# Kernel optimization log

Hardware: AMD Instinct MI355X
Metric: run time of the kernel (lower is better)

The kernel has to match this reference:

```python
import jax, jax.numpy as jnp
import numpy as np

B, S, D, H, HD = 2, 2048, 1024, 16, 64


def setup_inputs() -> dict:
    key = jax.random.key(0)
    ks = jax.random.split(key, 5)
    sc = 1.0 / np.sqrt(D)  # lecun-normal-ish scale for kernels
    return {
        "x": jax.random.normal(ks[0], (B, S, D), jnp.float32),
        "Wq": jax.random.normal(ks[1], (D, H, HD), jnp.float32) * sc,
        "bq": jnp.zeros((H, HD), jnp.float32),
        "Wk": jax.random.normal(ks[2], (D, H, HD), jnp.float32) * sc,
        "bk": jnp.zeros((H, HD), jnp.float32),
        "Wv": jax.random.normal(ks[3], (D, H, HD), jnp.float32) * sc,
        "bv": jnp.zeros((H, HD), jnp.float32),
        "Wo": jax.random.normal(ks[4], (H, HD, D), jnp.float32) * (1.0 / np.sqrt(H * HD)),
        "bo": jnp.zeros((D,), jnp.float32),
    }


def reference(x, Wq, bq, Wk, bk, Wv, bv, Wo, bo):
    # QKV projections: [B,S,D] x [D,H,Hd] -> [B,S,H,Hd]
    q = jnp.einsum("bsd,dhk->bshk", x, Wq) + bq
    k = jnp.einsum("bsd,dhk->bshk", x, Wk) + bk
    v = jnp.einsum("bsd,dhk->bshk", x, Wv) + bv
    depth = q.shape[-1]
    q = q / jnp.sqrt(jnp.asarray(depth, q.dtype))
    # attention weights [B,H,Sq,Sk]
    attn = jnp.einsum("bqhd,bkhd->bhqk", q, k)
    attn = jax.nn.softmax(attn, axis=-1)
    # weighted values [B,Sq,H,Hd]
    out = jnp.einsum("bhqk,bkhd->bqhd", attn, v)
    # output projection back to d_model
    return jnp.einsum("bqhd,hdm->bqm", out, Wo) + bo
```

## Files before the change

kernel.cpp:

```cpp
#include <hip/hip_runtime.h>


typedef __attribute__((ext_vector_type(8))) short short8;
typedef __attribute__((ext_vector_type(4))) float float4v;
typedef __attribute__((ext_vector_type(16))) float f32x16;
typedef __attribute__((ext_vector_type(2))) int int2v;

__device__ __forceinline__ void async16(void* lds, const void* g) {
  __builtin_amdgcn_global_load_lds(
      (__attribute__((address_space(1))) void*)(g),
      (__attribute__((address_space(3))) void*)(lds), 16, 0, 0);
}

__device__ __forceinline__ short f2bf(float f) {
  union { float f; unsigned u; } v;
  v.f = f;
  unsigned r = v.u + 0x7fffu + ((v.u >> 16) & 1u);
  return (short)(r >> 16);
}

#if __has_builtin(__builtin_amdgcn_cvt_pk_bf16_f32)
__device__ __forceinline__ unsigned pk2(float a, float b) {
  auto h = __builtin_amdgcn_cvt_pk_bf16_f32(a, b);
  unsigned u;
  __builtin_memcpy(&u, &h, 4);
  return u;
}
#else
__device__ __forceinline__ unsigned pk2(float a, float b) {
  return (unsigned)(unsigned short)f2bf(a) |
         ((unsigned)(unsigned short)f2bf(b) << 16);
}
#endif

#if __has_builtin(__builtin_amdgcn_exp2f)
__device__ __forceinline__ float fexp2(float x) { return __builtin_amdgcn_exp2f(x); }
#else
__device__ __forceinline__ float fexp2(float x) { return exp2f(x); }
#endif

__device__ __forceinline__ void plswap(unsigned& a, unsigned& b) {
#if __has_builtin(__builtin_amdgcn_permlane32_swap)
  int2v r = __builtin_amdgcn_permlane32_swap((int)a, (int)b, false, false);
  a = (unsigned)r[0];
  b = (unsigned)r[1];
#else
  unsigned ax = (unsigned)__shfl_xor((int)a, 32);
  unsigned bx = (unsigned)__shfl_xor((int)b, 32);
  bool hh = (threadIdx.x & 32) != 0;
  a = hh ? bx : a;
  b = hh ? b : ax;
#endif
}

__device__ __forceinline__ short8 mk8(unsigned a, unsigned b, unsigned c,
                                      unsigned d) {
  union { unsigned u[4]; short8 s; } r;
  r.u[0] = a; r.u[1] = b; r.u[2] = c; r.u[3] = d;
  return r.s;
}

__device__ __forceinline__ short8 cvt8(const float* __restrict__ g) {
  float4v a = *(const float4v*)(g);
  float4v b = *(const float4v*)(g + 4);
  union { unsigned u[4]; short8 s; } r;
  r.u[0] = pk2(a[0], a[1]);
  r.u[1] = pk2(a[2], a[3]);
  r.u[2] = pk2(b[0], b[1]);
  r.u[3] = pk2(b[2], b[3]);
  return r.s;
}

__device__ __forceinline__ void mfma_tile(const short* As, const short* Bs,
                                          float4v acc[4][4]) {
  int t = threadIdx.x, lane = t & 63, w = t >> 6, r = lane & 15, q = lane >> 4;
  int wr = (w >> 1) * 64, wc = (w & 1) * 64;
  short8 af[4], bfr[4];
#pragma unroll
  for (int mt = 0; mt < 4; mt++)
    af[mt] = *(const short8*)(As + (wr + mt * 16 + r) * 32 + q * 8);
#pragma unroll
  for (int nt = 0; nt < 4; nt++)
    bfr[nt] = *(const short8*)(Bs + (wc + nt * 16 + r) * 32 + q * 8);
#pragma unroll
  for (int mt = 0; mt < 4; mt++)
#pragma unroll
    for (int nt = 0; nt < 4; nt++)
      acc[mt][nt] = __builtin_amdgcn_mfma_f32_16x16x32_bf16(
          af[mt], bfr[nt], acc[mt][nt], 0, 0, 0);
}

__global__ __launch_bounds__(256) void convw_t3(
    const float* __restrict__ W0, const float* __restrict__ W1,
    const float* __restrict__ W2, short* __restrict__ dst) {
  __shared__ short tile[64][65];
  int z = blockIdx.z;
  const float* src = (z == 0) ? W0 : (z == 1) ? W1 : W2;
  short* d = dst + z * 1048576;
  int r0 = blockIdx.y * 64, c0 = blockIdx.x * 64;
  int t = threadIdx.x;
#pragma unroll
  for (int i = 0; i < 16; i++) {
    int e = i * 256 + t;
    int r = e >> 6, c = e & 63;
    tile[r][c] = f2bf(src[(r0 + r) * 1024 + c0 + c]);
  }
  __syncthreads();
#pragma unroll
  for (int i = 0; i < 16; i++) {
    int e = i * 256 + t;
    int r = e >> 6, c = e & 63;
    d[(c0 + r) * 1024 + r0 + c] = tile[c][r];
  }
}

__global__ __launch_bounds__(256) void convwo_t(
    const float* __restrict__ W, short* __restrict__ d) {
  __shared__ short tile[64][65];
  int r0 = blockIdx.y * 64, c0 = blockIdx.x * 64;
  int t = threadIdx.x;
#pragma unroll
  for (int i = 0; i < 16; i++) {
    int e = i * 256 + t;
    int r = e >> 6, c = e & 63;
    tile[r][c] = f2bf(W[(r0 + r) * 1024 + c0 + c]);
  }
  __syncthreads();
#pragma unroll
  for (int i = 0; i < 16; i++) {
    int e = i * 256 + t;
    int r = e >> 6, c = e & 63;
    d[(c0 + r) * 1024 + r0 + c] = tile[c][r];
  }
}

__global__ __launch_bounds__(256) void conv_x(
    const float* __restrict__ x, short* __restrict__ xb) {
  int i = (blockIdx.x * 256 + threadIdx.x) * 8;
  *(short8*)(xb + i) = cvt8(x + i);
}

__global__ __launch_bounds__(256, 2) void qkv_gemm_fast(
    const short* __restrict__ xb, const short* __restrict__ WT,
    const float* __restrict__ bq, const float* __restrict__ bk,
    const float* __restrict__ bv, short* __restrict__ Qd,
    short* __restrict__ Kd, short* __restrict__ Vt0, short* __restrict__ Vt1) {
  __shared__ __align__(16) short As[4096];
  __shared__ __align__(16) short Bs[4096];
  int z = blockIdx.z;
  int t = threadIdx.x;
  int m0, n0;
  if (z < 2) { m0 = blockIdx.y * 128; n0 = blockIdx.x * 128; }
  else       { m0 = blockIdx.x * 128; n0 = blockIdx.y * 128; }
  const short* Wz = WT + z * 1048576;
  const short* A = (z < 2) ? xb : Wz;
  const short* B = (z < 2) ? Wz : xb;
  float4v acc[4][4];
#pragma unroll
  for (int mt = 0; mt < 4; mt++)
#pragma unroll
    for (int nt = 0; nt < 4; nt++)
#pragma unroll
      for (int k = 0; k < 4; k++) acc[mt][nt][k] = 0.0f;

  for (int kt = 0; kt < 32; kt++) {
    int k0 = kt * 32;
    __syncthreads();
#pragma unroll
    for (int i = 0; i < 2; i++) {
      int p = i * 256 + t;
      int rr = p >> 2, cc = p & 3;
      async16(As + p * 8, A + (m0 + rr) * 1024 + k0 + cc * 8);
      async16(Bs + p * 8, B + (n0 + rr) * 1024 + k0 + cc * 8);
    }
    __syncthreads();
    mfma_tile(As, Bs, acc);
  }
  int lane = t & 63, w = t >> 6, r = lane & 15, q = lane >> 4;
  int wr = (w >> 1) * 64, wc = (w & 1) * 64;
  if (z < 2) {
    const float* bias = (z == 0) ? bq : bk;
    short* dst = (z == 0) ? Qd : Kd;
    float scale = (z == 0) ? 0.1803368801111204f : 1.0f;
#pragma unroll
    for (int mt = 0; mt < 4; mt++)
#pragma unroll
      for (int reg = 0; reg < 4; reg++) {
        int m = m0 + wr + mt * 16 + q * 4 + reg;
        int b = m >> 11, s = m & 2047;
#pragma unroll
        for (int nt = 0; nt < 4; nt++) {
          int n = n0 + wc + nt * 16 + r;
          int h = n >> 6, hd = n & 63;
          float v = (acc[mt][nt][reg] + bias[n]) * scale;
          dst[((b * 16 + h) << 17) + (s << 6) + hd] = f2bf(v);
        }
      }
  } else {
#pragma unroll
    for (int mt = 0; mt < 4; mt++)
#pragma unroll
      for (int reg = 0; reg < 4; reg++) {
        int mrow = m0 + wr + mt * 16 + q * 4 + reg;
        int h = mrow >> 6, hd = mrow & 63;
        float bias = bv[mrow];
#pragma unroll
        for (int nt = 0; nt < 4; nt++) {
          int n = n0 + wc + nt * 16 + r;
          int b = n >> 11, s = n & 2047;
          int idx = b * 16 + h;
          short* vp = (idx < 16) ? (Vt0 + idx * 131072)
                                 : (Vt1 + (idx - 16) * 131072);
          vp[(hd << 11) + s] = f2bf(acc[mt][nt][reg] + bias);
        }
      }
  }
}

__device__ __forceinline__ void stage_kv(short* Ksb, short* Vsb,
                                         const short* Kt, const short* Vt,
                                         int t) {
#pragma unroll
  for (int i = 0; i < 2; i++) {
    int p = i * 256 + t, rr = p >> 3, c = p & 7, cs = (c ^ (rr & 7)) * 8;
    async16(Ksb + p * 8, Kt + rr * 64 + cs);
    async16(Vsb + p * 8, Vt + rr * 2048 + cs);
  }
}

__global__ __launch_bounds__(256, 2) void attn_kernel(
    short* __restrict__ QO, const short* __restrict__ K,
    const short* __restrict__ V0, const short* __restrict__ V1) {
  __shared__ __align__(16) short Ks[2][4096];
  __shared__ __align__(16) short Vs[2][4096];
  __shared__ float sums[4][32];
  int id = blockIdx.x;
  int chunk = id >> 3;
  int bh = (id & 7) * 4 + (chunk >> 4);
  int qt = chunk & 15;
  int t = threadIdx.x, lane = t & 63, w = t >> 6;
  int l31 = lane & 31, hi = lane >> 5;
  short* Qb = QO + bh * 131072;
  const short* Kb = K + bh * 131072;
  const short* Vb = (bh < 16) ? (V0 + bh * 131072) : (V1 + (bh - 16) * 131072);
  int q0w = qt * 128 + w * 32;

  short8 qf[4];
#pragma unroll
  for (int ds = 0; ds < 4; ds++)
    qf[ds] = *(const short8*)(Qb + (q0w + l31) * 64 + ds * 16 + hi * 8);

  f32x16 oacc[2];
#pragma unroll
  for (int ht = 0; ht < 2; ht++)
#pragma unroll
    for (int i = 0; i < 16; i++) oacc[ht][i] = 0.0f;
  float lsum = 0.0f;

  stage_kv(Ks[0], Vs[0], Kb, Vb, t);
  __syncthreads();

  for (int kt = 0; kt < 32; kt++) {
    int cur = kt & 1;
    if (kt < 31)
      stage_kv(Ks[cur ^ 1], Vs[cur ^ 1], Kb + (kt + 1) * 4096,
               Vb + (kt + 1) * 64, t);
    const short* Kc = Ks[cur];
    const short* Vc = Vs[cur];
#pragma unroll
    for (int ck = 0; ck < 2; ck++) {
      int kr = ck * 32 + l31;
      short8 ka[4];
#pragma unroll
      for (int ds = 0; ds < 4; ds++)
        ka[ds] =
            *(const short8*)(Kc + kr * 64 + (((ds * 2 + hi) ^ (kr & 7)) * 8));
      f32x16 sacc;
#pragma unroll
      for (int i = 0; i < 16; i++) sacc[i] = 0.0f;
      __builtin_amdgcn_s_setprio(1);
#pragma unroll
      for (int ds = 0; ds < 4; ds++)
        sacc = __builtin_amdgcn_mfma_f32_32x32x16_bf16(ka[ds], qf[ds], sacc,
                                                       0, 0, 0);
      __builtin_amdgcn_s_setprio(0);
      float pv[16];
#pragma unroll
      for (int i = 0; i < 16; i++) pv[i] = fexp2(sacc[i]);
      lsum += (((pv[0] + pv[1]) + (pv[2] + pv[3])) +
               ((pv[4] + pv[5]) + (pv[6] + pv[7]))) +
              (((pv[8] + pv[9]) + (pv[10] + pv[11])) +
               ((pv[12] + pv[13]) + (pv[14] + pv[15])));
      unsigned u0 = pk2(pv[0], pv[1]), u1 = pk2(pv[2], pv[3]);
      unsigned u2 = pk2(pv[4], pv[5]), u3 = pk2(pv[6], pv[7]);
      unsigned u4 = pk2(pv[8], pv[9]), u5 = pk2(pv[10], pv[11]);
      unsigned u6 = pk2(pv[12], pv[13]), u7 = pk2(pv[14], pv[15]);
      plswap(u0, u2);
      plswap(u1, u3);
      plswap(u4, u6);
      plswap(u5, u7);
      short8 pa[2];
      pa[0] = mk8(u0, u1, u2, u3);
      pa[1] = mk8(u4, u5, u6, u7);
#pragma unroll
      for (int ks = 0; ks < 2; ks++) {
        short8 vb8[2];
#pragma unroll
        for (int ht = 0; ht < 2; ht++) {
          int d = ht * 32 + l31;
          vb8[ht] = *(const short8*)(Vc + d * 64 +
                                     (((ck * 4 + ks * 2 + hi) ^ (d & 7)) * 8));
        }
        __builtin_amdgcn_s_setprio(1);
#pragma unroll
        for (int ht = 0; ht < 2; ht++)
          oacc[ht] = __builtin_amdgcn_mfma_f32_32x32x16_bf16(
              pa[ks], vb8[ht], oacc[ht], 0, 0, 0);
        __builtin_amdgcn_s_setprio(0);
      }
    }
    __syncthreads();
  }

  {
    float lt = lsum + __shfl_xor(lsum, 32);
    float inv = 1.0f / fmaxf(lt, 1.0e-30f);
    if (lane < 32) sums[w][l31] = inv;
  }
  __builtin_amdgcn_s_waitcnt(0xC07F);
#pragma unroll
  for (int rg = 0; rg < 16; rg++) {
    int srow = (rg & 3) + 8 * (rg >> 2) + 4 * hi;
    float inv = sums[w][srow];
    short* orow = Qb + (q0w + srow) * 64;
    orow[l31] = f2bf(oacc[0][rg] * inv);
    orow[32 + l31] = f2bf(oacc[1][rg] * inv);
  }
}

__global__ __launch_bounds__(256, 2) void out_gemm(
    const short* __restrict__ O, const short* __restrict__ WoT,
    const float* __restrict__ bo, float* __restrict__ out) {
  __shared__ __align__(16) short As[4096];
  __shared__ __align__(16) short Bs[2048];
  int m0 = blockIdx.y * 128, n0 = blockIdx.x * 64;
  int t = threadIdx.x, lane = t & 63, w = t >> 6, r = lane & 15, q = lane >> 4;
  int wr = (w >> 1) * 64, wc = (w & 1) * 32;
  float4v acc[4][2];
#pragma unroll
  for (int mt = 0; mt < 4; mt++)
#pragma unroll
    for (int nt = 0; nt < 2; nt++)
#pragma unroll
      for (int k = 0; k < 4; k++) acc[mt][nt][k] = 0.0f;

  for (int kt = 0; kt < 32; kt++) {
    int k0 = kt * 32;
    int h0 = k0 >> 6, hd0 = k0 & 63;
    __syncthreads();
#pragma unroll
    for (int i = 0; i < 2; i++) {
      int p = i * 256 + t;
      int rr = p >> 2, cc = p & 3;
      int m = m0 + rr;
      async16(As + p * 8, O + (m >> 11) * 2097152 + h0 * 131072 +
                              (m & 2047) * 64 + hd0 + cc * 8);
    }
    {
      int rr = t >> 2, cc = t & 3;
      async16(Bs + t * 8, WoT + (n0 + rr) * 1024 + k0 + cc * 8);
    }
    __syncthreads();
    short8 af[4], bfr[2];
#pragma unroll
    for (int mt = 0; mt < 4; mt++)
      af[mt] = *(const short8*)(As + (wr + mt * 16 + r) * 32 + q * 8);
#pragma unroll
    for (int nt = 0; nt < 2; nt++)
      bfr[nt] = *(const short8*)(Bs + (wc + nt * 16 + r) * 32 + q * 8);
#pragma unroll
    for (int mt = 0; mt < 4; mt++)
#pragma unroll
      for (int nt = 0; nt < 2; nt++)
        acc[mt][nt] = __builtin_amdgcn_mfma_f32_16x16x32_bf16(
            af[mt], bfr[nt], acc[mt][nt], 0, 0, 0);
  }
#pragma unroll
  for (int mt = 0; mt < 4; mt++)
#pragma unroll
    for (int reg = 0; reg < 4; reg++) {
      int m = m0 + wr + mt * 16 + q * 4 + reg;
#pragma unroll
      for (int nt = 0; nt < 2; nt++) {
        int n = n0 + wc + nt * 16 + r;
        out[m * 1024 + n] = acc[mt][nt][reg] + bo[n];
      }
    }
}

extern "C" void kernel_launch(void* const* d_in, const int* in_sizes, int n_in,
                              void* d_out, int out_size, void* d_ws,
                              size_t ws_size, hipStream_t stream) {
  (void)in_sizes; (void)n_in; (void)out_size; (void)ws_size;
  const float* x = (const float*)d_in[0];
  const float* Wq = (const float*)d_in[1];
  const float* bq = (const float*)d_in[2];
  const float* Wk = (const float*)d_in[3];
  const float* bk = (const float*)d_in[4];
  const float* Wv = (const float*)d_in[5];
  const float* bv = (const float*)d_in[6];
  const float* Wo = (const float*)d_in[7];
  const float* bo = (const float*)d_in[8];
  float* out = (float*)d_out;
  char* ws = (char*)d_ws;
  short* QO  = (short*)(ws);
  short* Kws = (short*)(ws + (8u << 20));
  short* WoT = (short*)(ws + (8u << 20));
  short* xb  = (short*)d_out;
  short* WT  = (short*)d_out + 4 * 1048576;
  short* Vt0 = (short*)Wq;
  short* Vt1 = (short*)Wk;

  dim3 tb(256);
  convw_t3<<<dim3(16, 16, 3), tb, 0, stream>>>(Wq, Wk, Wv, WT);
  conv_x<<<dim3(2048), tb, 0, stream>>>(x, xb);
  qkv_gemm_fast<<<dim3(8, 32, 3), tb, 0, stream>>>(xb, WT, bq, bk, bv,
                                                   QO, Kws, Vt0, Vt1);
  attn_kernel<<<dim3(512), tb, 0, stream>>>(QO, Kws, Vt0, Vt1);
  convwo_t<<<dim3(16, 16), tb, 0, stream>>>(Wo, WoT);
  out_gemm<<<dim3(16, 32), tb, 0, stream>>>(QO, WoT, bo, out);
}
```

Before: 203.6 us.

## Split attention KV tiles across warp pairs and double the block count

Each attention block now covers 64 query rows instead of 128. Its four warps are split so that two warps handle the two 32-key halves of each KV tile for the same query rows. Partial outputs and row sums from the second half are reduced through LDS, which reuses the KV staging buffer, before normalization and the store. The grid doubles to 1024 blocks and launch bounds rise to 4 blocks per CU, aiming for more parallelism and occupancy, at the cost of loading each KV tile twice as often per query and an extra LDS reduction.

New measurement: 202.4 us. No clear change (-0.6%).

```diff
diff --git a/kernel.cpp b/kernel.cpp
--- a/kernel.cpp
+++ b/kernel.cpp
@@ -228,22 +228,24 @@
   }
 }
 
-__global__ __launch_bounds__(256, 2) void attn_kernel(
+__global__ __launch_bounds__(256, 4) void attn_kernel(
     short* __restrict__ QO, const short* __restrict__ K,
     const short* __restrict__ V0, const short* __restrict__ V1) {
-  __shared__ __align__(16) short Ks[2][4096];
-  __shared__ __align__(16) short Vs[2][4096];
-  __shared__ float sums[4][32];
+  __shared__ __align__(16) short SM[16640];
+  float* sums = (float*)(SM + 16384);
+  float* xl = (float*)(SM + 16512);
+  float* xo = (float*)SM;
   int id = blockIdx.x;
   int chunk = id >> 3;
-  int bh = (id & 7) * 4 + (chunk >> 4);
-  int qt = chunk & 15;
+  int bh = (id & 7) * 4 + (chunk >> 5);
+  int qt = chunk & 31;
   int t = threadIdx.x, lane = t & 63, w = t >> 6;
   int l31 = lane & 31, hi = lane >> 5;
+  int qsel = w & 1, kh = w >> 1;
   short* Qb = QO + bh * 131072;
   const short* Kb = K + bh * 131072;
   const short* Vb = (bh < 16) ? (V0 + bh * 131072) : (V1 + (bh - 16) * 131072);
-  int q0w = qt * 128 + w * 32;
+  int q0w = qt * 64 + qsel * 32;
 
   short8 qf[4];
 #pragma unroll
@@ -257,18 +259,18 @@
     for (int i = 0; i < 16; i++) oacc[ht][i] = 0.0f;
   float lsum = 0.0f;
 
-  stage_kv(Ks[0], Vs[0], Kb, Vb, t);
+  stage_kv(SM, SM + 8192, Kb, Vb, t);
   __syncthreads();
 
   for (int kt = 0; kt < 32; kt++) {
     int cur = kt & 1;
     if (kt < 31)
-      stage_kv(Ks[cur ^ 1], Vs[cur ^ 1], Kb + (kt + 1) * 4096,
-               Vb + (kt + 1) * 64, t);
-    const short* Kc = Ks[cur];
-    const short* Vc = Vs[cur];
-#pragma unroll
-    for (int ck = 0; ck < 2; ck++) {
+      stage_kv(SM + (cur ^ 1) * 4096, SM + 8192 + (cur ^ 1) * 4096,
+               Kb + (kt + 1) * 4096, Vb + (kt + 1) * 64, t);
+    const short* Kc = SM + cur * 4096;
+    const short* Vc = SM + 8192 + cur * 4096;
+    {
+      int ck = kh;
       int kr = ck * 32 + l31;
       short8 ka[4];
 #pragma unroll
@@ -322,19 +324,33 @@
     __syncthreads();
   }
 
-  {
-    float lt = lsum + __shfl_xor(lsum, 32);
-    float inv = 1.0f / fmaxf(lt, 1.0e-30f);
-    if (lane < 32) sums[w][l31] = inv;
-  }
-  __builtin_amdgcn_s_waitcnt(0xC07F);
-#pragma unroll
-  for (int rg = 0; rg < 16; rg++) {
-    int srow = (rg & 3) + 8 * (rg >> 2) + 4 * hi;
-    float inv = sums[w][srow];
-    short* orow = Qb + (q0w + srow) * 64;
-    orow[l31] = f2bf(oacc[0][rg] * inv);
-    orow[32 + l31] = f2bf(oacc[1][rg] * inv);
+  float lt = lsum + __shfl_xor(lsum, 32);
+  float* xb = xo + (qsel * 64 + lane) * 33;
+  if (kh == 1) {
+#pragma unroll
+    for (int i = 0; i < 16; i++) xb[i] = oacc[0][i];
+#pragma unroll
+    for (int i = 0; i < 16; i++) xb[16 + i] = oacc[1][i];
+    if (lane < 32) xl[qsel * 32 + l31] = lt;
+  }
+  __syncthreads();
+  if (kh == 0) {
+#pragma unroll
+    for (int i = 0; i < 16; i++) oacc[0][i] += xb[i];
+#pragma unroll
+    for (int i = 0; i < 16; i++) oacc[1][i] += xb[16 + i];
+    float ltot = lt + xl[qsel * 32 + l31];
+    float inv = 1.0f / fmaxf(ltot, 1.0e-30f);
+    if (lane < 32) sums[qsel * 32 + l31] = inv;
+    __builtin_amdgcn_s_waitcnt(0xC07F);
+#pragma unroll
+    for (int rg = 0; rg < 16; rg++) {
+      int srow = (rg & 3) + 8 * (rg >> 2) + 4 * hi;
+      float invr = sums[qsel * 32 + srow];
+      short* orow = Qb + (q0w + srow) * 64;
+      orow[l31] = f2bf(oacc[0][rg] * invr);
+      orow[32 + l31] = f2bf(oacc[1][rg] * invr);
+    }
   }
 }
 
@@ -426,7 +442,7 @@
   conv_x<<<dim3(2048), tb, 0, stream>>>(x, xb);
   qkv_gemm_fast<<<dim3(8, 32, 3), tb, 0, stream>>>(xb, WT, bq, bk, bv,
                                                    QO, Kws, Vt0, Vt1);
-  attn_kernel<<<dim3(512), tb, 0, stream>>>(QO, Kws, Vt0, Vt1);
+  attn_kernel<<<dim3(1024), tb, 0, stream>>>(QO, Kws, Vt0, Vt1);
   convwo_t<<<dim3(16, 16), tb, 0, stream>>>(Wo, WoT);
   out_gemm<<<dim3(16, 32), tb, 0, stream>>>(QO, WoT, bo, out);
 }
```
